# Kernel optimization log

Hardware: AMD Instinct MI355X
Metric: run time of the kernel (lower is better)

## Reference

```python
import jax, jax.numpy as jnp
import numpy as np

B, H, W = 64, 512, 512
T = 100           # num_thresholds
R = 8             # defect regions per image (max label id)
BLOCK = 128       # defect regions are 128x128 blocks on a 4x4 grid
SAT = 1.0         # saturation_threshold (relative)


def setup_inputs() -> dict:
    key = jax.random.key(0)
    k1, _ = jax.random.split(key)
    preds = jax.random.uniform(k1, (B, H, W), dtype=jnp.float32)
    thresholds = jnp.linspace(0.0, 1.0, T).astype(jnp.float32)
    # Build a labeled GT mask: R disjoint 128x128 block regions per image,
    # labels 1..R (0 = background). This plays the role of measure.label(target).
    rng = np.random.default_rng(0)
    labels = np.zeros((B, H, W), dtype=np.int32)
    gb = H // BLOCK           # 4 blocks per side -> 16 candidate blocks
    nblocks = gb * gb
    for b in range(B):
        chosen = rng.permutation(nblocks)[:R]
        for rid, blk in enumerate(chosen, start=1):
            r, c = divmod(int(blk), gb)
            labels[b, r * BLOCK:(r + 1) * BLOCK, c * BLOCK:(c + 1) * BLOCK] = rid
    return {"preds": preds, "thresholds": thresholds, "labels": jnp.asarray(labels)}


def reference(preds, thresholds, labels):
    # preds: (B,H,W) float32 in [0,1); thresholds: (T,) sorted; labels: (B,H,W) int32, 0=bg.
    Bn, Hn, Wn = preds.shape
    Tn = thresholds.shape[0]
    flat_s = preds.reshape(-1)
    flat_l = labels.reshape(-1)
    # bucket[p] = number of thresholds <= score[p]; pixel passes thr[t] iff bucket > t.
    bucket = jnp.searchsorted(thresholds, flat_s, side='right')  # int in [0, T]
    # ---- background FP / TN per threshold (exact counts via histogram) ----
    bg = (flat_l == 0).astype(jnp.int32)
    bg_hist = jax.ops.segment_sum(bg, bucket, num_segments=Tn + 1)  # (T+1,)
    bg_total = bg_hist.sum()
    fp = (bg_total - jnp.cumsum(bg_hist)[:Tn]).astype(jnp.float32)  # fp[t] = #bg with score>=thr[t]
    tn = bg_total.astype(jnp.float32) - fp
    # ---- per-region TP per threshold (segmented histogram) ----
    bidx = jnp.repeat(jnp.arange(Bn), Hn * Wn)
    seg = bidx * R + (flat_l - 1)              # region id in [0, B*R)
    comb = seg * (Tn + 1) + bucket
    NSEG = Bn * R * (Tn + 1)
    comb = jnp.where(flat_l > 0, comb, NSEG)   # dump bg pixels in overflow slot
    hist = jax.ops.segment_sum(jnp.ones_like(bucket, dtype=jnp.int32), comb,
                               num_segments=NSEG + 1)[:NSEG].reshape(Bn, R, Tn + 1)
    area = hist.sum(-1)                                       # (B,R) defect areas
    tp = (area[..., None] - jnp.cumsum(hist, -1)[..., :Tn]).astype(jnp.float32)  # (B,R,T)
    sat = jnp.maximum(area.astype(jnp.float32) * SAT, 1.0)    # relative saturation
    valid = (area > 0).astype(jnp.float32)                    # guard empty regions
    spro = jnp.minimum(tp / sat[..., None], 1.0) * valid[..., None]
    spro_sum = spro.sum((0, 1))                               # (T,)
    n_def = jnp.maximum(valid.sum(), 1.0)
    mean_spro = spro_sum / n_def
    # ---- AUC over FPR (max_fpr = 1.0) ----
    denom = fp + tn
    fpr = jnp.where(denom > 0, fp / jnp.maximum(denom, 1.0), 0.0)
    order = jnp.argsort(fpr)
    x = fpr[order]
    y = mean_spro[order]
    auc = jnp.sum((x[1:] - x[:-1]) * (y[1:] + y[:-1]) * 0.5)  # trapezoid rule
    return auc
```

## Files before the change

kernel.cpp:

```cpp
#include <hip/hip_runtime.h>

#define B_N 64
#define H_N 512
#define W_N 512
#define T_N 100
#define TB  101
#define R_N 8
#define NLAB 9
#define BLOCKS_PER_IMG 16
#define PIX_PER_IMG (H_N * W_N)
#define PIX_PER_BLOCK (PIX_PER_IMG / BLOCKS_PER_IMG)

__global__ __launch_bounds__(256) void hist_kernel(
    const float* __restrict__ preds, const int* __restrict__ labels,
    const float* __restrict__ thr,
    int* __restrict__ region_hist,
    int* __restrict__ bg_hist)
{
    __shared__ float s_thr[T_N];
    __shared__ int whist[4][NLAB * TB];

    const int tid  = threadIdx.x;
    const int wave = tid >> 6;

    for (int i = tid; i < 4 * NLAB * TB; i += 256) ((int*)whist)[i] = 0;
    if (tid < T_N) s_thr[tid] = thr[tid];
    __syncthreads();

    const int img   = blockIdx.x / BLOCKS_PER_IMG;
    const int chunk = blockIdx.x % BLOCKS_PER_IMG;
    const long base = (long)img * PIX_PER_IMG + (long)chunk * PIX_PER_BLOCK;
    const float4* p4 = (const float4*)(preds + base);
    const int4*   l4 = (const int4*)(labels + base);
    int* __restrict__ myh = whist[wave];

    const int iters = PIX_PER_BLOCK / (256 * 4);
    for (int it = 0; it < iters; ++it) {
        float4 pv = p4[it * 256 + tid];
        int4   lv = l4[it * 256 + tid];
        float ps[4] = {pv.x, pv.y, pv.z, pv.w};
        int   ls[4] = {lv.x, lv.y, lv.z, lv.w};
#pragma unroll
        for (int j = 0; j < 4; ++j) {
            float s = ps[j];
            int k = (int)(s * (float)(T_N - 1)) + 1;
            k = max(0, min(T_N, k));
            while (k < T_N && s_thr[k] <= s) ++k;
            while (k > 0 && s_thr[k - 1] > s) --k;
            atomicAdd(&myh[ls[j] * TB + k], 1);
        }
    }
    __syncthreads();

    for (int i = tid; i < NLAB * TB; i += 256) {
        int v = whist[0][i] + whist[1][i] + whist[2][i] + whist[3][i];
        if (v) {
            int lab = i / TB;
            int t   = i - lab * TB;
            if (lab == 0)
                atomicAdd(&bg_hist[img * TB + t], v);
            else
                atomicAdd(&region_hist[(img * R_N + (lab - 1)) * TB + t], v);
        }
    }
}

__global__ __launch_bounds__(128) void region_kernel(
    const int* __restrict__ region_hist,
    float* __restrict__ spro_sum,
    int* __restrict__ n_def)
{
    __shared__ float spro_sh[R_N][T_N];
    __shared__ int validc[R_N];
    const int img = blockIdx.x;
    const int tid = threadIdx.x;

    if (tid < R_N) {
        const int* h = &region_hist[(img * R_N + tid) * TB];
        int area = 0;
        for (int t = 0; t < TB; ++t) area += h[t];
        float sat   = fmaxf((float)area, 1.0f);
        float valid = (area > 0) ? 1.0f : 0.0f;
        int csum = 0;
        for (int t = 0; t < T_N; ++t) {
            csum += h[t];
            float tp = (float)(area - csum);
            spro_sh[tid][t] = fminf(tp / sat, 1.0f) * valid;
        }
        validc[tid] = (area > 0) ? 1 : 0;
    }
    __syncthreads();

    if (tid < T_N) {
        float s = 0.0f;
        for (int r = 0; r < R_N; ++r) s += spro_sh[r][tid];
        atomicAdd(&spro_sum[tid], s);
    }
    if (tid == 0) {
        int v = 0;
        for (int r = 0; r < R_N; ++r) v += validc[r];
        atomicAdd(n_def, v);
    }
}

__global__ __launch_bounds__(128) void final_kernel(
    const int* __restrict__ bg_hist,
    const float* __restrict__ spro_sum,
    const int* __restrict__ n_def,
    float* __restrict__ out)
{
    __shared__ int    bgh[TB];
    __shared__ float  fpr_sh[T_N];
    __shared__ float  ms_sh[T_N];
    __shared__ int    order[T_N];
    __shared__ double contrib[T_N];
    const int tid = threadIdx.x;

    if (tid < TB) {
        int s = 0;
        for (int b = 0; b < B_N; ++b) s += bg_hist[b * TB + tid];
        bgh[tid] = s;
    }
    __syncthreads();

    if (tid < T_N) {
        int fp_i = 0;
        for (int k = tid + 1; k < TB; ++k) fp_i += bgh[k];
        int tot = fp_i;
        for (int k = 0; k <= tid; ++k) tot += bgh[k];
        float bgt = (float)tot;
        float fp  = (float)fp_i;
        fpr_sh[tid] = (bgt > 0.0f) ? fp / fmaxf(bgt, 1.0f) : 0.0f;
        float nd = fmaxf((float)(*n_def), 1.0f);
        ms_sh[tid] = spro_sum[tid] / nd;
    }
    __syncthreads();

    if (tid < T_N) {
        float v = fpr_sh[tid];
        int r = 0;
        for (int j = 0; j < T_N; ++j) {
            float u = fpr_sh[j];
            r += (u < v) | ((u == v) & (j < tid));
        }
        order[r] = tid;
    }
    __syncthreads();

    if (tid < T_N - 1) {
        int o0 = order[tid], o1 = order[tid + 1];
        double x0 = fpr_sh[o0], x1 = fpr_sh[o1];
        double y0 = ms_sh[o0],  y1 = ms_sh[o1];
        contrib[tid] = (x1 - x0) * (y0 + y1) * 0.5;
    } else if (tid < T_N) {
        contrib[tid] = 0.0;
    }
    __syncthreads();

    if (tid == 0) {
        double s = 0.0;
        for (int i = 0; i < T_N - 1; ++i) s += contrib[i];
        out[0] = (float)s;
    }
}

extern "C" void kernel_launch(void* const* d_in, const int* in_sizes, int n_in,
                              void* d_out, int out_size, void* d_ws, size_t ws_size,
                              hipStream_t stream) {
    const float* preds  = (const float*)d_in[0];
    const float* thr    = (const float*)d_in[1];
    const int*   labels = (const int*)d_in[2];
    float* out = (float*)d_out;

    int*   region_hist = (int*)d_ws;
    int*   bg_hist     = region_hist + B_N * R_N * TB;
    float* spro_sum    = (float*)(bg_hist + B_N * TB);
    int*   n_def       = (int*)(spro_sum + T_N);

    size_t zbytes = sizeof(int) * (size_t)(B_N * R_N * TB + B_N * TB)
                  + sizeof(float) * T_N + sizeof(int);
    hipMemsetAsync(d_ws, 0, zbytes, stream);

    hist_kernel<<<B_N * BLOCKS_PER_IMG, 256, 0, stream>>>(preds, labels, thr,
                                                          region_hist, bg_hist);
    region_kernel<<<B_N, 128, 0, stream>>>(region_hist, spro_sum, n_def);
    final_kernel<<<1, 128, 0, stream>>>(bg_hist, spro_sum, n_def, out);
}
```

Measured before the change: 167.1 us.

## Fuse region and final kernels via last-block ticket; double hist grid and batch loads

The histogram kernel now splits each image into 32 chunks instead of 16, giving 2048 blocks with an occupancy hint. Each thread issues four float4/int4 loads at a time before processing them, which exposes more memory-level parallelism. The region and final kernels are merged into one launch: a last-block-done atomic ticket runs the AUC computation, and the background histogram is accumulated with atomics. This removes one kernel launch and the serial 64-image sum, at the cost of more global atomics and more per-block histogram init/flush overhead.

```diff
diff --git a/kernel.cpp b/kernel.cpp
--- a/kernel.cpp
+++ b/kernel.cpp
@@ -7,11 +7,11 @@
 #define TB  101
 #define R_N 8
 #define NLAB 9
-#define BLOCKS_PER_IMG 16
+#define CHUNKS 32
 #define PIX_PER_IMG (H_N * W_N)
-#define PIX_PER_BLOCK (PIX_PER_IMG / BLOCKS_PER_IMG)
-
-__global__ __launch_bounds__(256) void hist_kernel(
+#define CPIX (PIX_PER_IMG / CHUNKS)
+
+__global__ __launch_bounds__(256, 8) void hist_kernel(
     const float* __restrict__ preds, const int* __restrict__ labels,
     const float* __restrict__ thr,
     int* __restrict__ region_hist,
@@ -27,27 +27,35 @@
     if (tid < T_N) s_thr[tid] = thr[tid];
     __syncthreads();
 
-    const int img   = blockIdx.x / BLOCKS_PER_IMG;
-    const int chunk = blockIdx.x % BLOCKS_PER_IMG;
-    const long base = (long)img * PIX_PER_IMG + (long)chunk * PIX_PER_BLOCK;
+    const int img   = blockIdx.x >> 5;
+    const int chunk = blockIdx.x & (CHUNKS - 1);
+    const long base = (long)img * PIX_PER_IMG + (long)chunk * CPIX;
     const float4* p4 = (const float4*)(preds + base);
     const int4*   l4 = (const int4*)(labels + base);
     int* __restrict__ myh = whist[wave];
 
-    const int iters = PIX_PER_BLOCK / (256 * 4);
-    for (int it = 0; it < iters; ++it) {
-        float4 pv = p4[it * 256 + tid];
-        int4   lv = l4[it * 256 + tid];
-        float ps[4] = {pv.x, pv.y, pv.z, pv.w};
-        int   ls[4] = {lv.x, lv.y, lv.z, lv.w};
-#pragma unroll
-        for (int j = 0; j < 4; ++j) {
-            float s = ps[j];
-            int k = (int)(s * (float)(T_N - 1)) + 1;
-            k = max(0, min(T_N, k));
-            while (k < T_N && s_thr[k] <= s) ++k;
-            while (k > 0 && s_thr[k - 1] > s) --k;
-            atomicAdd(&myh[ls[j] * TB + k], 1);
+#pragma unroll
+    for (int g = 0; g < 2; ++g) {
+        float4 pv[4];
+        int4   lv[4];
+#pragma unroll
+        for (int u = 0; u < 4; ++u) {
+            pv[u] = p4[(g * 4 + u) * 256 + tid];
+            lv[u] = l4[(g * 4 + u) * 256 + tid];
+        }
+#pragma unroll
+        for (int u = 0; u < 4; ++u) {
+            float ps[4] = {pv[u].x, pv[u].y, pv[u].z, pv[u].w};
+            int   ls[4] = {lv[u].x, lv[u].y, lv[u].z, lv[u].w};
+#pragma unroll
+            for (int j = 0; j < 4; ++j) {
+                float s = ps[j];
+                int k = (int)(s * (float)(T_N - 1)) + 1;
+                k = max(0, min(T_N, k));
+                while (k < T_N && s_thr[k] <= s) ++k;
+                while (k > 0 && s_thr[k - 1] > s) --k;
+                atomicAdd(&myh[ls[j] * TB + k], 1);
+            }
         }
     }
     __syncthreads();
@@ -65,15 +73,22 @@
     }
 }
 
-__global__ __launch_bounds__(128) void region_kernel(
+__global__ __launch_bounds__(128) void region_final_kernel(
     const int* __restrict__ region_hist,
+    const int* __restrict__ bg_hist,
     float* __restrict__ spro_sum,
-    int* __restrict__ n_def)
+    int* __restrict__ n_def,
+    int* __restrict__ bgh_total,
+    int* __restrict__ done_ctr,
+    float* __restrict__ out)
 {
     __shared__ float spro_sh[R_N][T_N];
     __shared__ int validc[R_N];
+    __shared__ int s_ticket;
     const int img = blockIdx.x;
     const int tid = threadIdx.x;
+
+    if (tid < TB) atomicAdd(&bgh_total[tid], bg_hist[img * TB + tid]);
 
     if (tid < R_N) {
         const int* h = &region_hist[(img * R_N + tid) * TB];
@@ -101,26 +116,31 @@
         for (int r = 0; r < R_N; ++r) v += validc[r];
         atomicAdd(n_def, v);
     }
-}
-
-__global__ __launch_bounds__(128) void final_kernel(
-    const int* __restrict__ bg_hist,
-    const float* __restrict__ spro_sum,
-    const int* __restrict__ n_def,
-    float* __restrict__ out)
-{
+
+    __threadfence();
+    if (tid == 0)
+        s_ticket = __hip_atomic_fetch_add(done_ctr, 1, __ATOMIC_ACQ_REL,
+                                          __HIP_MEMORY_SCOPE_AGENT);
+    __syncthreads();
+    if (s_ticket != B_N - 1) return;
+
     __shared__ int    bgh[TB];
+    __shared__ float  s_spro[T_N];
     __shared__ float  fpr_sh[T_N];
     __shared__ float  ms_sh[T_N];
     __shared__ int    order[T_N];
     __shared__ double contrib[T_N];
-    const int tid = threadIdx.x;
-
-    if (tid < TB) {
-        int s = 0;
-        for (int b = 0; b < B_N; ++b) s += bg_hist[b * TB + tid];
-        bgh[tid] = s;
-    }
+    __shared__ int    s_nd;
+
+    if (tid < TB)
+        bgh[tid] = __hip_atomic_load(&bgh_total[tid], __ATOMIC_RELAXED,
+                                     __HIP_MEMORY_SCOPE_AGENT);
+    if (tid < T_N)
+        s_spro[tid] = __hip_atomic_load(&spro_sum[tid], __ATOMIC_RELAXED,
+                                        __HIP_MEMORY_SCOPE_AGENT);
+    if (tid == 0)
+        s_nd = __hip_atomic_load(n_def, __ATOMIC_RELAXED,
+                                 __HIP_MEMORY_SCOPE_AGENT);
     __syncthreads();
 
     if (tid < T_N) {
@@ -131,8 +151,8 @@
         float bgt = (float)tot;
         float fp  = (float)fp_i;
         fpr_sh[tid] = (bgt > 0.0f) ? fp / fmaxf(bgt, 1.0f) : 0.0f;
-        float nd = fmaxf((float)(*n_def), 1.0f);
-        ms_sh[tid] = spro_sum[tid] / nd;
+        float nd = fmaxf((float)s_nd, 1.0f);
+        ms_sh[tid] = s_spro[tid] / nd;
     }
     __syncthreads();
 
@@ -174,15 +194,17 @@
 
     int*   region_hist = (int*)d_ws;
     int*   bg_hist     = region_hist + B_N * R_N * TB;
-    float* spro_sum    = (float*)(bg_hist + B_N * TB);
+    int*   bgh_total   = bg_hist + B_N * TB;
+    float* spro_sum    = (float*)(bgh_total + TB);
     int*   n_def       = (int*)(spro_sum + T_N);
-
-    size_t zbytes = sizeof(int) * (size_t)(B_N * R_N * TB + B_N * TB)
-                  + sizeof(float) * T_N + sizeof(int);
+    int*   done_ctr    = n_def + 1;
+
+    size_t zbytes = sizeof(int) * (size_t)(B_N * R_N * TB + B_N * TB + TB)
+                  + sizeof(float) * T_N + 2 * sizeof(int);
     hipMemsetAsync(d_ws, 0, zbytes, stream);
 
-    hist_kernel<<<B_N * BLOCKS_PER_IMG, 256, 0, stream>>>(preds, labels, thr,
-                                                          region_hist, bg_hist);
-    region_kernel<<<B_N, 128, 0, stream>>>(region_hist, spro_sum, n_def);
-    final_kernel<<<1, 128, 0, stream>>>(bg_hist, spro_sum, n_def, out);
+    hist_kernel<<<B_N * CHUNKS, 256, 0, stream>>>(preds, labels, thr,
+                                                  region_hist, bg_hist);
+    region_final_kernel<<<B_N, 128, 0, stream>>>(region_hist, bg_hist, spro_sum,
+                                                 n_def, bgh_total, done_ctr, out);
 }
```

Result: slower. 172.5 us (+3.2%).
